# Optimization experiments

Hardware: AMD Instinct MI355X
Metric: run time of the kernel (lower is better)

## Reference

```python
import jax, jax.numpy as jnp
import numpy as np

N_NODE = 200000   # item catalog size (n_node)
EMB = 100         # emb_size
NNZ = 1000000     # hypergraph adjacency nonzeros
B = 1024          # batch / cl_size
L = 50            # session length
LAYERS = 2        # HyperConv layers (opt.layer)
TAU = 0.2         # contrastive temperature
K_NEI = 3         # FindNeighbors.neighbor_n


def setup_inputs() -> dict:
    key = jax.random.key(0)
    ks = jax.random.split(key, 16)
    g = 1.414 / np.sqrt(EMB)  # xavier_normal gain=1.414 scale
    inp = {}
    inp["embedding"] = jax.random.normal(ks[0], (N_NODE, EMB), jnp.float32) * 0.1
    inp["adj_val"] = jax.random.uniform(ks[1], (NNZ,), jnp.float32)
    inp["A"] = jax.random.uniform(ks[2], (B, B), jnp.float32) * 0.01
    inp["D"] = jax.random.uniform(ks[3], (B, B), jnp.float32) * 0.01
    inp["z2"] = jax.random.normal(ks[4], (B, EMB), jnp.float32)
    inp["Wcf1"] = jax.random.normal(ks[5], (EMB, EMB), jnp.float32) * g
    inp["bcf1"] = jnp.zeros((EMB,), jnp.float32)
    inp["Wcf2"] = jax.random.normal(ks[6], (EMB, EMB), jnp.float32) * g
    inp["bcf2"] = jnp.zeros((EMB,), jnp.float32)
    inp["Wkg1"] = jax.random.normal(ks[7], (EMB, EMB), jnp.float32) * g
    inp["bkg1"] = jnp.zeros((EMB,), jnp.float32)
    inp["Wkg2"] = jax.random.normal(ks[8], (EMB, EMB), jnp.float32) * g
    inp["bkg2"] = jnp.zeros((EMB,), jnp.float32)
    inp["session_len"] = jnp.full((B, 1), float(L), jnp.float32)
    inp["adj_row"] = jax.random.randint(ks[9], (NNZ,), 0, N_NODE, jnp.int32)
    inp["adj_col"] = jax.random.randint(ks[10], (NNZ,), 0, N_NODE, jnp.int32)
    inp["items"] = jax.random.randint(ks[11], (B, L), 0, N_NODE + 1, jnp.int32)
    return inp


def _proj(z, W1, b1, W2, b2):
    # nn.Linear -> ELU -> nn.Linear (Contrast_2view projector)
    return jax.nn.elu(z @ W1.T + b1) @ W2.T + b2


def reference(embedding, adj_val, A, D, z2,
              Wcf1, bcf1, Wcf2, bcf2, Wkg1, bkg1, Wkg2, bkg2,
              session_len, adj_row, adj_col, items):
    # ---- HyperConv: layered sparse propagation, averaged over layers ----
    h = embedding
    acc = embedding
    for _ in range(LAYERS):
        # torch.sparse.mm(adjacency, h) via gather + segment_sum
        h = jax.ops.segment_sum(adj_val[:, None] * h[adj_col], adj_row,
                                num_segments=N_NODE)
        acc = acc + h
    hyper = acc / (LAYERS + 1)  # [N_NODE, EMB]

    # ---- RelationGAT.forward ----
    emb_pad = jnp.concatenate([jnp.zeros((1, EMB), hyper.dtype), hyper], axis=0)
    seq_h = emb_pad[items]                       # [B, L, EMB]
    rel = jnp.sum(seq_h, axis=1) / session_len   # [B, EMB]
    rel = (D @ A) @ rel                          # session-graph conv
    c = jax.nn.selu(rel)
    l_c = c / jnp.linalg.norm(c, axis=-1, keepdims=True)  # [B, EMB]

    # ---- FindNeighbors (dropout omitted: eval mode) ----
    sess = l_c
    norms = jnp.sqrt(jnp.sum(sess * sess + 1e-6, axis=1, keepdims=True))
    cos = (sess @ sess.T) / (norms @ norms.T)    # [B, B]
    cos = jax.nn.softmax(cos, axis=-1)
    topv, topi = jax.lax.top_k(cos, K_NEI)       # [B, K]
    topv = jax.nn.softmax(topv, axis=-1)
    neighbor = jnp.sum(topv[:, :, None] * sess[topi], axis=1)  # [B, EMB]

    # ---- Contrast_2view ----
    z1p = _proj(sess, Wcf1, bcf1, Wcf2, bcf2)
    z2p = _proj(z2, Wkg1, bkg1, Wkg2, bkg2)
    n1 = jnp.linalg.norm(z1p, axis=-1, keepdims=True)
    n2 = jnp.linalg.norm(z2p, axis=-1, keepdims=True)
    simm = jnp.exp((z1p @ z2p.T) / (n1 @ n2.T) / TAU)
    simm = simm / (jnp.sum(simm, axis=1, keepdims=True) + 1e-8)
    cl_loss = -jnp.mean(jnp.log(jnp.diagonal(simm)))  # pos = eye

    return hyper, l_c, neighbor, cl_loss
```

## Files before the change

### kernel.cpp

```cpp
#include <hip/hip_runtime.h>
#include <hip/hip_bf16.h>

#define N_NODE 200000
#define EMB 100
#define NNZ 1000000
#define BATCH 1024
#define SLEN 50
#define BE (BATCH * EMB)
#define SCAN_BLK 1024
#define PROJ_ROWS 8
#define UNR 8

#define OFF_LC    20000000LL
#define OFF_NB    20102400LL
#define OFF_LOSS  20204800LL

typedef __hip_bfloat16 bf16;

__device__ __forceinline__ float b2f(bf16 x) { return __bfloat162float(x); }
__device__ __forceinline__ bf16 f2b(float x) { return __float2bfloat16(x); }

__device__ __forceinline__ float ldf(const void* p, long long i, int f32) {
    return f32 ? ((const float*)p)[i] : b2f(((const bf16*)p)[i]);
}
__device__ __forceinline__ void stf(void* p, long long i, int f32, float v) {
    if (f32) ((float*)p)[i] = v;
    else     ((bf16*)p)[i] = f2b(v);
}

__device__ __forceinline__ float bfb2f(unsigned short s) {
    return __uint_as_float(((unsigned)s) << 16);
}
__device__ __forceinline__ unsigned short f2bfb(float x) {
    bf16 h = f2b(x); unsigned short r; __builtin_memcpy(&r, &h, 2); return r;
}
__device__ __forceinline__ float2 up2(unsigned u) {
    return make_float2(bfb2f((unsigned short)(u & 0xffff)), bfb2f((unsigned short)(u >> 16)));
}
__device__ __forceinline__ unsigned pk2(float a, float b) {
    return (unsigned)f2bfb(a) | ((unsigned)f2bfb(b) << 16);
}
__device__ __forceinline__ float2 ldf2(const void* p, long long pi, int f32) {
    if (f32) return ((const float2*)p)[pi];
    return up2(((const unsigned*)p)[pi]);
}
template<bool F32>
__device__ __forceinline__ float2 ldf2t(const void* p, long long pi) {
    if (F32) return ((const float2*)p)[pi];
    return up2(((const unsigned*)p)[pi]);
}
__device__ __forceinline__ void stf2(void* p, long long pi, int f32, float a, float b) {
    if (f32) ((float2*)p)[pi] = make_float2(a, b);
    else     ((unsigned*)p)[pi] = pk2(a, b);
}

__device__ __forceinline__ float wave_allreduce_sum(float v) {
    for (int m = 32; m > 0; m >>= 1) v += __shfl_xor(v, m, 64);
    return v;
}

__global__ void hist_kernel(const int* __restrict__ rows, int* __restrict__ counts,
                            const void* __restrict__ adjval, int* __restrict__ flag) {
    if (blockIdx.x == 0 && threadIdx.x == 0) {
        int f = 0;
        const bf16* p = (const bf16*)adjval;
        for (int i = 0; i < 64; i++) {
            float x = b2f(p[i]);
            if (!(x >= 0.0f && x <= 1.0f)) f = 1;
        }
        *flag = f;
    }
    int e = blockIdx.x * 256 + threadIdx.x;
    if (e < NNZ) atomicAdd(&counts[rows[e]], 1);
}

__global__ void scan_block(const int* __restrict__ counts, int* __restrict__ incl,
                           int* __restrict__ bsums) {
    __shared__ int s[SCAN_BLK];
    int i = blockIdx.x * SCAN_BLK + threadIdx.x;
    int v = (i < N_NODE) ? counts[i] : 0;
    s[threadIdx.x] = v;
    __syncthreads();
    for (int off = 1; off < SCAN_BLK; off <<= 1) {
        int add = (threadIdx.x >= (unsigned)off) ? s[threadIdx.x - off] : 0;
        __syncthreads();
        s[threadIdx.x] += add;
        __syncthreads();
    }
    if (i < N_NODE) incl[i] = s[threadIdx.x];
    if (threadIdx.x == SCAN_BLK - 1) bsums[blockIdx.x] = s[threadIdx.x];
}

__global__ void scan_add(const int* __restrict__ counts, const int* __restrict__ incl,
                         const int* __restrict__ bsums, int* __restrict__ row_ptr,
                         int* __restrict__ cursor, int nb) {
    __shared__ int s[256];
    int t = threadIdx.x;
    if (t < 256) s[t] = (t < nb) ? bsums[t] : 0;
    __syncthreads();
    for (int off = 1; off < 256; off <<= 1) {
        int add = 0;
        if (t < 256 && t >= off) add = s[t - off];
        __syncthreads();
        if (t < 256) s[t] += add;
        __syncthreads();
    }
    int base = (blockIdx.x == 0) ? 0 : s[blockIdx.x - 1];
    int i = blockIdx.x * SCAN_BLK + t;
    if (i < N_NODE) {
        int ex = incl[i] - counts[i] + base;
        row_ptr[i] = ex;
        cursor[i] = ex;
    }
    if (i == 0) row_ptr[N_NODE] = NNZ;
}

__global__ void permute_edges(const int* __restrict__ arow, const int* __restrict__ acol,
                              const void* __restrict__ aval, int* __restrict__ cursor,
                              int2* __restrict__ cv, const int* __restrict__ flagp) {
    const int f32 = *flagp;
    int e = blockIdx.x * 256 + threadIdx.x;
    if (blockIdx.x == 0 && threadIdx.x < 8) cv[NNZ + threadIdx.x] = make_int2(0, 0);
    if (e >= NNZ) return;
    int r = arow[e];
    int pos = atomicAdd(&cursor[r], 1);
    float v = ldf(aval, e, f32);
    cv[pos] = make_int2(acol[e], __float_as_int(v));
}

__global__ __launch_bounds__(256) void repack_emb(const void* __restrict__ emb,
                                                  void* __restrict__ embp, int f32) {
    long long idx = (long long)blockIdx.x * 256 + threadIdx.x;
    if (idx >= (long long)N_NODE * 64) return;
    long long r = idx >> 6;
    int l = (int)(idx & 63);
    float2 v = make_float2(0.f, 0.f);
    if (l < 50) v = ldf2(emb, r * 50 + l, f32);
    stf2(embp, r * 64 + l, f32, v.x, v.y);
}

__device__ __forceinline__ void ld_cv8(int2* c, const int2* __restrict__ cv, int k0) {
    #pragma unroll
    for (int j = 0; j < UNR; j++) c[j] = cv[k0 + j];
}

template<bool F32>
__device__ __forceinline__ void spmm1_body(
        const int* __restrict__ rp, const int2* __restrict__ cv,
        const void* __restrict__ src, int estride, unsigned* __restrict__ h1) {
    int lane = threadIdx.x & 63;
    int r = blockIdx.x * 4 + (threadIdx.x >> 6);
    if (r >= N_NODE) return;
    bool act = lane < 50;
    int pl = (estride == 64) ? lane : (act ? lane : 0);
    int k0 = rp[r], k1 = rp[r + 1];
    int2 c[UNR];
    ld_cv8(c, cv, k0);
    int c0x = c[0].x;
    float2 e[UNR];
    #pragma unroll
    for (int j = 0; j < UNR; j++) {
        int cl = (k0 + j < k1) ? c[j].x : c0x;
        e[j] = ldf2t<F32>(src, (long long)cl * estride + pl);
    }
    float a0 = 0.f, a1 = 0.f;
    #pragma unroll
    for (int j = 0; j < UNR; j++) {
        float v = (k0 + j < k1) ? __int_as_float(c[j].y) : 0.f;
        a0 += v * e[j].x; a1 += v * e[j].y;
    }
    for (int k = k0 + UNR; k < k1; k += UNR) {
        int2 ct[UNR];
        #pragma unroll
        for (int j = 0; j < UNR; j++) { int kk = k + j; ct[j] = cv[kk < k1 ? kk : k1 - 1]; }
        float2 et[UNR];
        #pragma unroll
        for (int j = 0; j < UNR; j++)
            et[j] = ldf2t<F32>(src, (long long)ct[j].x * estride + pl);
        #pragma unroll
        for (int j = 0; j < UNR; j++) {
            float v = (k + j < k1) ? __int_as_float(ct[j].y) : 0.f;
            a0 += v * et[j].x; a1 += v * et[j].y;
        }
    }
    h1[(long long)r * 64 + lane] = pk2(a0, a1);
}

__global__ __launch_bounds__(256) void spmm_gather1(
        const int* __restrict__ rp, const int2* __restrict__ cv,
        const void* __restrict__ src, int estride,
        unsigned* __restrict__ h1, const int* __restrict__ flagp) {
    if (*flagp) spmm1_body<true>(rp, cv, src, estride, h1);
    else        spmm1_body<false>(rp, cv, src, estride, h1);
}

template<bool F32>
__device__ __forceinline__ void spmm2_body(
        const int* __restrict__ rp, const int2* __restrict__ cv,
        const void* __restrict__ emb,
        const unsigned* __restrict__ h1, void* __restrict__ out) {
    int lane = threadIdx.x & 63;
    int r = blockIdx.x * 4 + (threadIdx.x >> 6);
    if (r >= N_NODE) return;
    bool act = lane < 50;
    int pl = act ? lane : 0;
    int k0 = rp[r], k1 = rp[r + 1];
    int2 c[UNR];
    ld_cv8(c, cv, k0);
    int c0x = c[0].x;
    float2 ebv = ldf2t<F32>(emb, (long long)r * 50 + pl);
    float2 h1r = up2(h1[(long long)r * 64 + lane]);
    float2 e[UNR];
    #pragma unroll
    for (int j = 0; j < UNR; j++) {
        int cl = (k0 + j < k1) ? c[j].x : c0x;
        e[j] = up2(h1[(long long)cl * 64 + lane]);
    }
    float a0 = 0.f, a1 = 0.f;
    #pragma unroll
    for (int j = 0; j < UNR; j++) {
        float v = (k0 + j < k1) ? __int_as_float(c[j].y) : 0.f;
        a0 += v * e[j].x; a1 += v * e[j].y;
    }
    for (int k = k0 + UNR; k < k1; k += UNR) {
        int2 ct[UNR];
        #pragma unroll
        for (int j = 0; j < UNR; j++) { int kk = k + j; ct[j] = cv[kk < k1 ? kk : k1 - 1]; }
        float2 et[UNR];
        #pragma unroll
        for (int j = 0; j < UNR; j++)
            et[j] = up2(h1[(long long)ct[j].x * 64 + lane]);
        #pragma unroll
        for (int j = 0; j < UNR; j++) {
            float v = (k + j < k1) ? __int_as_float(ct[j].y) : 0.f;
            a0 += v * et[j].x; a1 += v * et[j].y;
        }
    }
    if (act)
        stf2(out, (long long)r * 50 + lane, F32 ? 1 : 0,
             (ebv.x + h1r.x + a0) * (1.0f / 3.0f), (ebv.y + h1r.y + a1) * (1.0f / 3.0f));
}

__global__ __launch_bounds__(256) void spmm_gather2(
        const int* __restrict__ rp, const int2* __restrict__ cv,
        const void* __restrict__ emb,
        const unsigned* __restrict__ h1, void* __restrict__ out,
        const int* __restrict__ flagp) {
    if (*flagp) spmm2_body<true>(rp, cv, emb, h1, out);
    else        spmm2_body<false>(rp, cv, emb, h1, out);
}

template<bool F32>
__device__ __forceinline__ void rel_rows_body(
        const void* __restrict__ out, const int* __restrict__ items,
        const void* __restrict__ slen, float* __restrict__ rel) {
    int lane = threadIdx.x & 63;
    int b = blockIdx.x * 4 + (threadIdx.x >> 6);
    if (b >= BATCH || lane >= 50) return;
    float s0 = 0.f, s1 = 0.f;
    #pragma unroll
    for (int l0 = 0; l0 < SLEN; l0 += 10) {
        int it[10];
        #pragma unroll
        for (int j = 0; j < 10; j++) it[j] = items[b * SLEN + l0 + j];
        float2 e[10];
        #pragma unroll
        for (int j = 0; j < 10; j++) {
            int idx = (it[j] > 0) ? it[j] - 1 : 0;
            e[j] = ldf2t<F32>(out, (long long)idx * 50 + lane);
        }
        #pragma unroll
        for (int j = 0; j < 10; j++) {
            float m = (it[j] > 0) ? 1.f : 0.f;
            s0 += m * e[j].x; s1 += m * e[j].y;
        }
    }
    float inv = 1.0f / ldf(slen, b, F32 ? 1 : 0);
    ((float2*)rel)[b * 50 + lane] = make_float2(s0 * inv, s1 * inv);
}

__global__ __launch_bounds__(256) void rel_rows(
        const void* __restrict__ out, const int* __restrict__ items,
        const void* __restrict__ slen, float* __restrict__ rel,
        const int* __restrict__ flagp) {
    if (*flagp) rel_rows_body<true>(out, items, slen, rel);
    else        rel_rows_body<false>(out, items, slen, rel);
}

__device__ __forceinline__ void bmm0_dev(float* smem, const void* __restrict__ M,
                                         const float* __restrict__ X, float* __restrict__ Y,
                                         int f32, int blk) {
    float (*ms)[BATCH] = (float(*)[BATCH])smem;
    int i0 = blk * 4;
    int t = threadIdx.x;
    for (int idx = t; idx < 4 * BATCH; idx += 256) {
        int rr = idx >> 10, j = idx & 1023;
        ms[rr][j] = ldf(M, (long long)(i0 + rr) * BATCH + j, f32);
    }
    __syncthreads();
    int w = t >> 6, lane = t & 63;
    if (lane >= 50) return;
    int i = i0 + w;
    const float2* X2 = (const float2*)X;
    float s0 = 0.f, s1 = 0.f;
    for (int j = 0; j < BATCH; j++) {
        float m = ms[w][j];
        float2 x = X2[j * 50 + lane];
        s0 += m * x.x; s1 += m * x.y;
    }
    ((float2*)Y)[i * 50 + lane] = make_float2(s0, s1);
}

__device__ void proj_dev(float* smem, const void* __restrict__ X, int x_dual,
                         const void* __restrict__ W1, const void* __restrict__ B1,
                         const void* __restrict__ W2, const void* __restrict__ B2,
                         float* __restrict__ Z, float* __restrict__ ZT,
                         float* __restrict__ nrm, int f32, int blk) {
    float* wT = smem;
    float* bsh = smem + 10000;
    float (*hid)[EMB] = (float(*)[EMB])(smem + 10100);
    float (*xr)[EMB]  = (float(*)[EMB])(smem + 10900);
    float (*red2)[2]  = (float(*)[2])(smem + 11100);
    int t = threadIdx.x;
    int sub = t >> 7, u = t & 127;
    int r0 = blk * PROJ_ROWS;
    for (int idx = t; idx < EMB * EMB; idx += 256) {
        int o = idx / EMB, k = idx - o * EMB;
        wT[k * EMB + o] = ldf(W1, idx, f32);
    }
    if (t < EMB) bsh[t] = ldf(B1, t, f32);
    __syncthreads();
    for (int pr = 0; pr < PROJ_ROWS; pr += 2) {
        int row = r0 + pr + sub;
        if (u < EMB)
            xr[sub][u] = x_dual ? ldf(X, (long long)row * EMB + u, f32)
                                : ((const float*)X)[row * EMB + u];
        __syncthreads();
        if (u < EMB) {
            float s = bsh[u];
            for (int k = 0; k < EMB; k++) s += xr[sub][k] * wT[k * EMB + u];
            hid[pr + sub][u] = (s > 0.f) ? s : expm1f(s);
        }
        __syncthreads();
    }
    for (int idx = t; idx < EMB * EMB; idx += 256) {
        int o = idx / EMB, k = idx - o * EMB;
        wT[k * EMB + o] = ldf(W2, idx, f32);
    }
    if (t < EMB) bsh[t] = ldf(B2, t, f32);
    __syncthreads();
    for (int pr = 0; pr < PROJ_ROWS; pr += 2) {
        int row = r0 + pr + sub;
        float sq = 0.f;
        if (u < EMB) {
            float o = bsh[u];
            const float* h = hid[pr + sub];
            for (int k = 0; k < EMB; k++) o += h[k] * wT[k * EMB + u];
            Z[(long long)row * EMB + u] = o;
            if (ZT) ZT[(long long)u * BATCH + row] = o;
            sq = o * o;
        }
        sq = wave_allreduce_sum(sq);
        if ((t & 63) == 0) red2[sub][(t >> 6) & 1] = sq;
        __syncthreads();
        if (u == 0) nrm[row] = sqrtf(red2[sub][0] + red2[sub][1]);
        __syncthreads();
    }
}

__global__ __launch_bounds__(256) void bmm1_projz2(
        const void* __restrict__ A, const float* __restrict__ relv, float* __restrict__ t1,
        const void* __restrict__ z2,
        const void* __restrict__ W1, const void* __restrict__ B1,
        const void* __restrict__ W2, const void* __restrict__ B2,
        float* __restrict__ z2p, float* __restrict__ z2pT, float* __restrict__ n2,
        const int* __restrict__ flagp) {
    __shared__ float smem[11104];
    const int f32 = *flagp;
    if (blockIdx.x < 256) bmm0_dev(smem, A, relv, t1, f32, blockIdx.x);
    else proj_dev(smem, z2, 1, W1, B1, W2, B2, z2p, z2pT, n2, f32, blockIdx.x - 256);
}

__global__ __launch_bounds__(256) void bmm2_selu(const void* __restrict__ M,
                                                 const float* __restrict__ X,
                                                 float* __restrict__ sess,
                                                 float* __restrict__ sessT,
                                                 float* __restrict__ ns,
                                                 void* __restrict__ out,
                                                 float* __restrict__ lacc,
                                                 int* __restrict__ done,
                                                 const int* __restrict__ flagp) {
    __shared__ float ms[4][BATCH];
    const int f32 = *flagp;
    if (blockIdx.x == 0 && threadIdx.x == 0) { *lacc = 0.f; *done = 0; }
    int i0 = blockIdx.x * 4;
    int t = threadIdx.x;
    for (int idx = t; idx < 4 * BATCH; idx += 256) {
        int rr = idx >> 10, j = idx & 1023;
        ms[rr][j] = ldf(M, (long long)(i0 + rr) * BATCH + j, f32);
    }
    __syncthreads();
    int w = t >> 6, lane = t & 63;
    bool act = lane < 50;
    int i = i0 + w;
    float s0 = 0.f, s1 = 0.f;
    if (act) {
        const float2* X2 = (const float2*)X;
        for (int j = 0; j < BATCH; j++) {
            float m = ms[w][j];
            float2 x = X2[j * 50 + lane];
            s0 += m * x.x; s1 += m * x.y;
        }
    }
    const float sc = 1.0507009873554804934193349852946f;
    const float al = 1.6732632423543772848170429916717f;
    float c0 = (s0 > 0.f) ? sc * s0 : sc * (al * expm1f(s0));
    float c1 = (s1 > 0.f) ? sc * s1 : sc * (al * expm1f(s1));
    if (!act) { c0 = 0.f; c1 = 0.f; }
    float nrm = sqrtf(wave_allreduce_sum(c0 * c0 + c1 * c1));
    float l0 = c0 / nrm, l1 = c1 / nrm;
    float nterm = act ? (l0 * l0 + l1 * l1 + 2e-6f) : 0.f;
    float n2sum = wave_allreduce_sum(nterm);
    if (act) {
        ((float2*)sess)[i * 50 + lane] = make_float2(l0, l1);
        sessT[(2 * lane) * BATCH + i] = l0;
        sessT[(2 * lane + 1) * BATCH + i] = l1;
        stf2(out, OFF_LC / 2 + (long long)i * 50 + lane, f32, l0, l1);
    }
    if (lane == 0) ns[i] = sqrtf(n2sum);
}

__global__ void neighbor_kernel(const float* __restrict__ sess, const float* __restrict__ sessT,
                                const float* __restrict__ ns, void* __restrict__ out,
                                const int* __restrict__ flagp) {
    __shared__ float si[EMB];
    __shared__ float red[4];
    __shared__ float wrv[4]; __shared__ int wri[4];
    __shared__ float chv[3]; __shared__ int chi[3];
    __shared__ float stv[3];
    const int f32 = *flagp;
    int i = blockIdx.x, t = threadIdx.x;
    if (t < EMB) si[t] = sess[i * EMB + t];
    __syncthreads();
    float ni = ns[i];
    float d0 = 0.f, d1 = 0.f, d2 = 0.f, d3 = 0.f;
    for (int k = 0; k < EMB; k++) {
        float sv = si[k];
        const float* row = sessT + k * BATCH;
        d0 += sv * row[t];
        d1 += sv * row[t + 256];
        d2 += sv * row[t + 512];
        d3 += sv * row[t + 768];
    }
    float pv0 = expf(d0 / (ni * ns[t]));
    float pv1 = expf(d1 / (ni * ns[t + 256]));
    float pv2 = expf(d2 / (ni * ns[t + 512]));
    float pv3 = expf(d3 / (ni * ns[t + 768]));
    float local = pv0 + pv1 + pv2 + pv3;
    float w = wave_allreduce_sum(local);
    if ((t & 63) == 0) red[t >> 6] = w;
    __syncthreads();
    float S = red[0] + red[1] + red[2] + red[3];

    int c0 = -1, c1 = -1, c2 = -1;
    float pv[4] = {pv0, pv1, pv2, pv3};
    for (int r = 0; r < 3; r++) {
        float bv = -1e30f; int bi = 0x7fffffff;
        #pragma unroll
        for (int m = 0; m < 4; m++) {
            int j = t + (m << 8);
            if (j == c0 || j == c1 || j == c2) continue;
            float v = pv[m];
            if (v > bv || (v == bv && j < bi)) { bv = v; bi = j; }
        }
        #pragma unroll
        for (int off = 1; off < 64; off <<= 1) {
            float ov = __shfl_xor(bv, off);
            int oi = __shfl_xor(bi, off);
            if (ov > bv || (ov == bv && oi < bi)) { bv = ov; bi = oi; }
        }
        if ((t & 63) == 0) { wrv[t >> 6] = bv; wri[t >> 6] = bi; }
        __syncthreads();
        if (t == 0) {
            float fv = wrv[0]; int fi = wri[0];
            for (int wq = 1; wq < 4; wq++) {
                if (wrv[wq] > fv || (wrv[wq] == fv && wri[wq] < fi)) { fv = wrv[wq]; fi = wri[wq]; }
            }
            chv[r] = fv; chi[r] = fi;
        }
        __syncthreads();
        if (r == 0) c0 = chi[0];
        else if (r == 1) c1 = chi[1];
        else c2 = chi[2];
    }
    if (t == 0) {
        float e0 = expf(chv[0] / S), e1 = expf(chv[1] / S), e2 = expf(chv[2] / S);
        float es = e0 + e1 + e2;
        stv[0] = e0 / es; stv[1] = e1 / es; stv[2] = e2 / es;
    }
    __syncthreads();
    if (t < EMB) {
        float o = stv[0] * sess[chi[0] * EMB + t]
                + stv[1] * sess[chi[1] * EMB + t]
                + stv[2] * sess[chi[2] * EMB + t];
        stf(out, OFF_NB + i * EMB + t, f32, o);
    }
}

__global__ __launch_bounds__(256) void proj_z1(
        const void* __restrict__ X,
        const void* __restrict__ W1, const void* __restrict__ B1,
        const void* __restrict__ W2, const void* __restrict__ B2,
        float* __restrict__ Z, float* __restrict__ nrm,
        const int* __restrict__ flagp) {
    __shared__ float smem[11104];
    proj_dev(smem, X, 0, W1, B1, W2, B2, Z, nullptr, nrm, *flagp, blockIdx.x);
}

__global__ void loss_kernel(const float* __restrict__ z1p, const float* __restrict__ z2pT,
                            const float* __restrict__ n1, const float* __restrict__ n2,
                            float* __restrict__ acc, int* __restrict__ done,
                            void* __restrict__ out, const int* __restrict__ flagp) {
    __shared__ float zi[EMB];
    __shared__ float red[4];
    __shared__ float sdiag;
    const int f32 = *flagp;
    int i = blockIdx.x, t = threadIdx.x;
    if (t < EMB) zi[t] = z1p[i * EMB + t];
    __syncthreads();
    float ni = n1[i];
    float d0 = 0.f, d1 = 0.f, d2 = 0.f, d3 = 0.f;
    for (int k = 0; k < EMB; k++) {
        float zv = zi[k];
        const float* row = z2pT + k * BATCH;
        d0 += zv * row[t];
        d1 += zv * row[t + 256];
        d2 += zv * row[t + 512];
        d3 += zv * row[t + 768];
    }
    float e0 = expf(d0 / (ni * n2[t]) * 5.0f);
    float e1 = expf(d1 / (ni * n2[t + 256]) * 5.0f);
    float e2 = expf(d2 / (ni * n2[t + 512]) * 5.0f);
    float e3 = expf(d3 / (ni * n2[t + 768]) * 5.0f);
    if (t == (i & 255)) {
        int m = i >> 8;
        sdiag = (m == 0) ? e0 : (m == 1) ? e1 : (m == 2) ? e2 : e3;
    }
    float local = e0 + e1 + e2 + e3;
    float w = wave_allreduce_sum(local);
    if ((t & 63) == 0) red[t >> 6] = w;
    __syncthreads();
    if (t == 0) {
        float S = red[0] + red[1] + red[2] + red[3];
        float l = -logf(sdiag / (S + 1e-8f));
        atomicAdd(acc, l * (1.0f / BATCH));
        __threadfence();
        int old = atomicAdd(done, 1);
        if (old == (int)gridDim.x - 1) {
            float v = atomicAdd(acc, 0.0f);
            stf(out, OFF_LOSS, f32, v);
        }
    }
}

extern "C" void kernel_launch(void* const* d_in, const int* in_sizes, int n_in,
                              void* d_out, int out_size, void* d_ws, size_t ws_size,
                              hipStream_t stream) {
    const void* emb  = d_in[0];
    const void* aval = d_in[1];
    const void* Amat = d_in[2];
    const void* Dmat = d_in[3];
    const void* z2   = d_in[4];
    const void* Wcf1 = d_in[5];
    const void* bcf1 = d_in[6];
    const void* Wcf2 = d_in[7];
    const void* bcf2 = d_in[8];
    const void* Wkg1 = d_in[9];
    const void* bkg1 = d_in[10];
    const void* Wkg2 = d_in[11];
    const void* bkg2 = d_in[12];
    const void* slen = d_in[13];
    const int* arow  = (const int*)d_in[14];
    const int* acol  = (const int*)d_in[15];
    const int* items = (const int*)d_in[16];

    long long esz = in_sizes ? (long long)in_sizes[0] : 0;
    int f32_host = (esz == (long long)N_NODE * EMB * 4) ? 1 : 0;
    int known_dtype = (esz == (long long)N_NODE * EMB * 2) || f32_host;

    int* flag      = (int*)d_ws;
    int* counts    = (int*)((char*)d_ws + 256);
    int* cursor    = counts;
    int* row_ptr   = counts + N_NODE;
    int* bsums     = row_ptr + N_NODE + 64;
    int2* cv       = (int2*)(bsums + 256);
    int* scanbuf   = (int*)cv;
    unsigned* h1buf = (unsigned*)(cv + NNZ + 8);
    char* tailbase = (char*)(h1buf + (long long)N_NODE * 64);
    void* emb_pad  = (void*)tailbase;
    long long embpad_bytes = (long long)N_NODE * 64 * (f32_host ? 8 : 4);
    float* fsmall  = (float*)tailbase;
    float* rel   = fsmall;
    float* t1    = rel  + BE;
    float* sess  = t1   + BE;
    float* sessT = sess + BE;
    float* z1p   = sessT + BE;
    float* z2p   = z1p  + BE;
    float* z2pT  = z2p  + BE;
    float* ns    = z2pT + BE;
    float* n1    = ns + BATCH;
    float* n2    = n1 + BATCH;
    float* lacc  = n2 + BATCH;
    int*   done  = (int*)(lacc + 1);
    long long fsmall_bytes = ((char*)(done + 16)) - (char*)tailbase;
    long long base_off = tailbase - (char*)d_ws;
    long long need_pad = base_off + (embpad_bytes > fsmall_bytes ? embpad_bytes : fsmall_bytes);
    int use_pad = known_dtype && ((long long)ws_size >= need_pad);
    int estride = use_pad ? 64 : 50;

    const int nscan = (N_NODE + SCAN_BLK - 1) / SCAN_BLK;

    hipMemsetAsync(counts, 0, (size_t)N_NODE * sizeof(int), stream);
    hist_kernel<<<(NNZ + 255) / 256, 256, 0, stream>>>(arow, counts, aval, flag);
    scan_block<<<nscan, SCAN_BLK, 0, stream>>>(counts, scanbuf, bsums);
    scan_add<<<nscan, SCAN_BLK, 0, stream>>>(counts, scanbuf, bsums, row_ptr, cursor, nscan);
    permute_edges<<<(NNZ + 255) / 256, 256, 0, stream>>>(arow, acol, aval, cursor,
                                                         cv, flag);

    if (use_pad) {
        long long tot = (long long)N_NODE * 64;
        repack_emb<<<(unsigned)((tot + 255) / 256), 256, 0, stream>>>(emb, emb_pad, f32_host);
        spmm_gather1<<<(N_NODE + 3) / 4, 256, 0, stream>>>(row_ptr, cv, emb_pad, estride,
                                                           h1buf, flag);
    } else {
        spmm_gather1<<<(N_NODE + 3) / 4, 256, 0, stream>>>(row_ptr, cv, emb, estride,
                                                           h1buf, flag);
    }
    spmm_gather2<<<(N_NODE + 3) / 4, 256, 0, stream>>>(row_ptr, cv, emb, h1buf,
                                                       d_out, flag);

    rel_rows<<<(BATCH + 3) / 4, 256, 0, stream>>>(d_out, items, slen, rel, flag);
    bmm1_projz2<<<384, 256, 0, stream>>>(Amat, rel, t1,
                                         z2, Wkg1, bkg1, Wkg2, bkg2,
                                         z2p, z2pT, n2, flag);
    bmm2_selu<<<BATCH / 4, 256, 0, stream>>>(Dmat, t1, sess, sessT, ns, d_out,
                                             lacc, done, flag);

    neighbor_kernel<<<BATCH, 256, 0, stream>>>(sess, sessT, ns, d_out, flag);

    proj_z1<<<BATCH / PROJ_ROWS, 256, 0, stream>>>(sess, Wcf1, bcf1, Wcf2, bcf2,
                                                   z1p, n1, flag);
    loss_kernel<<<BATCH, 256, 0, stream>>>(z1p, z2pT, n1, n2, lacc, done, d_out, flag);
}
```

Measured before the change: 711.5 us.

## Fuse histogram with embedding repack, vectorize edge kernels, merge neighbor/proj launches

Merges the row histogram and the embedding repack into one launch, and merges neighbor search with the z1 projection into one launch, cutting launch count. The histogram and permute kernels now handle four edges per thread using int4/float4 loads. The SpMM gathers switch to nontemporal loads for embedding and h1 rows, which changes how those gathered rows are cached. The cost is more divergent block roles within a launch, and the nontemporal hint may hurt reuse of gathered rows.

After: 737.0 us. 3.6% more time.

```diff
diff --git a/kernel.cpp b/kernel.cpp
--- a/kernel.cpp
+++ b/kernel.cpp
@@ -10,6 +10,7 @@
 #define SCAN_BLK 1024
 #define PROJ_ROWS 8
 #define UNR 8
+#define HIST_BLOCKS 977
 
 #define OFF_LC    20000000LL
 #define OFF_NB    20102400LL
@@ -49,6 +50,17 @@
     if (F32) return ((const float2*)p)[pi];
     return up2(((const unsigned*)p)[pi]);
 }
+template<bool F32>
+__device__ __forceinline__ float2 ldnt2(const void* p, long long pi) {
+    if (F32) {
+        unsigned long long u = __builtin_nontemporal_load((const unsigned long long*)p + pi);
+        return make_float2(__uint_as_float((unsigned)u), __uint_as_float((unsigned)(u >> 32)));
+    }
+    return up2(__builtin_nontemporal_load((const unsigned*)p + pi));
+}
+__device__ __forceinline__ float2 ldnt_h1(const unsigned* p, long long pi) {
+    return up2(__builtin_nontemporal_load(p + pi));
+}
 __device__ __forceinline__ void stf2(void* p, long long pi, int f32, float a, float b) {
     if (f32) ((float2*)p)[pi] = make_float2(a, b);
     else     ((unsigned*)p)[pi] = pk2(a, b);
@@ -59,8 +71,10 @@
     return v;
 }
 
-__global__ void hist_kernel(const int* __restrict__ rows, int* __restrict__ counts,
-                            const void* __restrict__ adjval, int* __restrict__ flag) {
+__global__ void hist_repack(const int* __restrict__ rows, int* __restrict__ counts,
+                            const void* __restrict__ adjval, int* __restrict__ flag,
+                            const void* __restrict__ emb, void* __restrict__ embp,
+                            int f32h) {
     if (blockIdx.x == 0 && threadIdx.x == 0) {
         int f = 0;
         const bf16* p = (const bf16*)adjval;
@@ -70,8 +84,24 @@
         }
         *flag = f;
     }
-    int e = blockIdx.x * 256 + threadIdx.x;
-    if (e < NNZ) atomicAdd(&counts[rows[e]], 1);
+    if (blockIdx.x < HIST_BLOCKS) {
+        int e0 = (blockIdx.x * 256 + threadIdx.x) * 4;
+        if (e0 < NNZ) {
+            int4 r4 = *(const int4*)&rows[e0];
+            atomicAdd(&counts[r4.x], 1);
+            atomicAdd(&counts[r4.y], 1);
+            atomicAdd(&counts[r4.z], 1);
+            atomicAdd(&counts[r4.w], 1);
+        }
+        return;
+    }
+    long long idx = (long long)(blockIdx.x - HIST_BLOCKS) * 256 + threadIdx.x;
+    if (idx >= (long long)N_NODE * 64) return;
+    long long r = idx >> 6;
+    int l = (int)(idx & 63);
+    float2 v = make_float2(0.f, 0.f);
+    if (l < 50) v = ldf2(emb, r * 50 + l, f32h);
+    stf2(embp, r * 64 + l, f32h, v.x, v.y);
 }
 
 __global__ void scan_block(const int* __restrict__ counts, int* __restrict__ incl,
@@ -119,24 +149,28 @@
                               const void* __restrict__ aval, int* __restrict__ cursor,
                               int2* __restrict__ cv, const int* __restrict__ flagp) {
     const int f32 = *flagp;
-    int e = blockIdx.x * 256 + threadIdx.x;
     if (blockIdx.x == 0 && threadIdx.x < 8) cv[NNZ + threadIdx.x] = make_int2(0, 0);
-    if (e >= NNZ) return;
-    int r = arow[e];
-    int pos = atomicAdd(&cursor[r], 1);
-    float v = ldf(aval, e, f32);
-    cv[pos] = make_int2(acol[e], __float_as_int(v));
-}
-
-__global__ __launch_bounds__(256) void repack_emb(const void* __restrict__ emb,
-                                                  void* __restrict__ embp, int f32) {
-    long long idx = (long long)blockIdx.x * 256 + threadIdx.x;
-    if (idx >= (long long)N_NODE * 64) return;
-    long long r = idx >> 6;
-    int l = (int)(idx & 63);
-    float2 v = make_float2(0.f, 0.f);
-    if (l < 50) v = ldf2(emb, r * 50 + l, f32);
-    stf2(embp, r * 64 + l, f32, v.x, v.y);
+    int e0 = (blockIdx.x * 256 + threadIdx.x) * 4;
+    if (e0 >= NNZ) return;
+    int4 r4 = *(const int4*)&arow[e0];
+    int4 c4 = *(const int4*)&acol[e0];
+    float v[4];
+    if (f32) {
+        float4 f = *(const float4*)((const float*)aval + e0);
+        v[0] = f.x; v[1] = f.y; v[2] = f.z; v[3] = f.w;
+    } else {
+        const unsigned* p = (const unsigned*)aval;
+        unsigned u0 = p[e0 >> 1], u1 = p[(e0 >> 1) + 1];
+        float2 a = up2(u0), b = up2(u1);
+        v[0] = a.x; v[1] = a.y; v[2] = b.x; v[3] = b.y;
+    }
+    int rr[4] = {r4.x, r4.y, r4.z, r4.w};
+    int cc[4] = {c4.x, c4.y, c4.z, c4.w};
+    #pragma unroll
+    for (int j = 0; j < 4; j++) {
+        int pos = atomicAdd(&cursor[rr[j]], 1);
+        cv[pos] = make_int2(cc[j], __float_as_int(v[j]));
+    }
 }
 
 __device__ __forceinline__ void ld_cv8(int2* c, const int2* __restrict__ cv, int k0) {
@@ -161,7 +195,7 @@
     #pragma unroll
     for (int j = 0; j < UNR; j++) {
         int cl = (k0 + j < k1) ? c[j].x : c0x;
-        e[j] = ldf2t<F32>(src, (long long)cl * estride + pl);
+        e[j] = ldnt2<F32>(src, (long long)cl * estride + pl);
     }
     float a0 = 0.f, a1 = 0.f;
     #pragma unroll
@@ -176,7 +210,7 @@
         float2 et[UNR];
         #pragma unroll
         for (int j = 0; j < UNR; j++)
-            et[j] = ldf2t<F32>(src, (long long)ct[j].x * estride + pl);
+            et[j] = ldnt2<F32>(src, (long long)ct[j].x * estride + pl);
         #pragma unroll
         for (int j = 0; j < UNR; j++) {
             float v = (k + j < k1) ? __int_as_float(ct[j].y) : 0.f;
@@ -214,7 +248,7 @@
     #pragma unroll
     for (int j = 0; j < UNR; j++) {
         int cl = (k0 + j < k1) ? c[j].x : c0x;
-        e[j] = up2(h1[(long long)cl * 64 + lane]);
+        e[j] = ldnt_h1(h1, (long long)cl * 64 + lane);
     }
     float a0 = 0.f, a1 = 0.f;
     #pragma unroll
@@ -229,7 +263,7 @@
         float2 et[UNR];
         #pragma unroll
         for (int j = 0; j < UNR; j++)
-            et[j] = up2(h1[(long long)ct[j].x * 64 + lane]);
+            et[j] = ldnt_h1(h1, (long long)ct[j].x * 64 + lane);
         #pragma unroll
         for (int j = 0; j < UNR; j++) {
             float v = (k + j < k1) ? __int_as_float(ct[j].y) : 0.f;
@@ -430,16 +464,17 @@
     if (lane == 0) ns[i] = sqrtf(n2sum);
 }
 
-__global__ void neighbor_kernel(const float* __restrict__ sess, const float* __restrict__ sessT,
-                                const float* __restrict__ ns, void* __restrict__ out,
-                                const int* __restrict__ flagp) {
-    __shared__ float si[EMB];
-    __shared__ float red[4];
-    __shared__ float wrv[4]; __shared__ int wri[4];
-    __shared__ float chv[3]; __shared__ int chi[3];
-    __shared__ float stv[3];
-    const int f32 = *flagp;
-    int i = blockIdx.x, t = threadIdx.x;
+__device__ void neighbor_dev(float* smem, const float* __restrict__ sess,
+                             const float* __restrict__ sessT, const float* __restrict__ ns,
+                             void* __restrict__ out, int f32, int i) {
+    float* si  = smem;
+    float* red = smem + 100;
+    float* wrv = smem + 104;
+    int*   wri = (int*)(smem + 108);
+    float* chv = smem + 112;
+    int*   chi = (int*)(smem + 115);
+    float* stv = smem + 118;
+    int t = threadIdx.x;
     if (t < EMB) si[t] = sess[i * EMB + t];
     __syncthreads();
     float ni = ns[i];
@@ -507,14 +542,18 @@
     }
 }
 
-__global__ __launch_bounds__(256) void proj_z1(
-        const void* __restrict__ X,
+__global__ __launch_bounds__(256) void neighbor_projz1(
+        const float* __restrict__ sess, const float* __restrict__ sessT,
+        const float* __restrict__ ns, void* __restrict__ out,
         const void* __restrict__ W1, const void* __restrict__ B1,
         const void* __restrict__ W2, const void* __restrict__ B2,
-        float* __restrict__ Z, float* __restrict__ nrm,
+        float* __restrict__ z1p, float* __restrict__ n1,
         const int* __restrict__ flagp) {
     __shared__ float smem[11104];
-    proj_dev(smem, X, 0, W1, B1, W2, B2, Z, nullptr, nrm, *flagp, blockIdx.x);
+    const int f32 = *flagp;
+    if (blockIdx.x < BATCH) neighbor_dev(smem, sess, sessT, ns, out, f32, blockIdx.x);
+    else proj_dev(smem, sess, 0, W1, B1, W2, B2, z1p, nullptr, n1, f32,
+                  blockIdx.x - BATCH);
 }
 
 __global__ void loss_kernel(const float* __restrict__ z1p, const float* __restrict__ z2pT,
@@ -619,17 +658,16 @@
     int estride = use_pad ? 64 : 50;
 
     const int nscan = (N_NODE + SCAN_BLK - 1) / SCAN_BLK;
+    const int repack_blocks = use_pad ? (int)(((long long)N_NODE * 64 + 255) / 256) : 0;
 
     hipMemsetAsync(counts, 0, (size_t)N_NODE * sizeof(int), stream);
-    hist_kernel<<<(NNZ + 255) / 256, 256, 0, stream>>>(arow, counts, aval, flag);
+    hist_repack<<<HIST_BLOCKS + repack_blocks, 256, 0, stream>>>(
+        arow, counts, aval, flag, emb, emb_pad, f32_host);
     scan_block<<<nscan, SCAN_BLK, 0, stream>>>(counts, scanbuf, bsums);
     scan_add<<<nscan, SCAN_BLK, 0, stream>>>(counts, scanbuf, bsums, row_ptr, cursor, nscan);
-    permute_edges<<<(NNZ + 255) / 256, 256, 0, stream>>>(arow, acol, aval, cursor,
-                                                         cv, flag);
+    permute_edges<<<HIST_BLOCKS, 256, 0, stream>>>(arow, acol, aval, cursor, cv, flag);
 
     if (use_pad) {
-        long long tot = (long long)N_NODE * 64;
-        repack_emb<<<(unsigned)((tot + 255) / 256), 256, 0, stream>>>(emb, emb_pad, f32_host);
         spmm_gather1<<<(N_NODE + 3) / 4, 256, 0, stream>>>(row_ptr, cv, emb_pad, estride,
                                                            h1buf, flag);
     } else {
@@ -646,9 +684,8 @@
     bmm2_selu<<<BATCH / 4, 256, 0, stream>>>(Dmat, t1, sess, sessT, ns, d_out,
                                              lacc, done, flag);
 
-    neighbor_kernel<<<BATCH, 256, 0, stream>>>(sess, sessT, ns, d_out, flag);
-
-    proj_z1<<<BATCH / PROJ_ROWS, 256, 0, stream>>>(sess, Wcf1, bcf1, Wcf2, bcf2,
-                                                   z1p, n1, flag);
+    neighbor_projz1<<<BATCH + BATCH / PROJ_ROWS, 256, 0, stream>>>(
+        sess, sessT, ns, d_out, Wcf1, bcf1, Wcf2, bcf2, z1p, n1, flag);
+
     loss_kernel<<<BATCH, 256, 0, stream>>>(z1p, z2pT, n1, n2, lacc, done, d_out, flag);
 }
```
